# Kernel tuning notes

Measured on AMD Instinct MI355X. Metric: run time of the kernel, lower is better.

The kernel has to match this reference:

```python
import jax, jax.numpy as jnp
import numpy as np

N = 50000        # nodes
E = 800000       # edges (avg degree 16)
F_IN = 128
H = 128
C = 16


def setup_inputs() -> dict:
    key = jax.random.key(0)
    ks = jax.random.split(key, 12)
    x = jax.random.normal(ks[0], (N, F_IN), dtype=jnp.float32)
    edges = jax.random.randint(ks[1], (2, E), 0, N, dtype=jnp.int32)
    dims = [(F_IN, H), (H, H // 2), (H // 2, H // 4), (H // 4, H // 8), (H // 8, C)]
    params = {}
    for i, (di, do) in enumerate(dims):
        params[f"W{i+1}"] = jax.random.normal(ks[2 + 2 * i], (di, do), dtype=jnp.float32) * (1.0 / np.sqrt(di)).astype(np.float32)
        params[f"b{i+1}"] = jax.random.normal(ks[3 + 2 * i], (do,), dtype=jnp.float32) * 0.01
    return {"x": x, "edges": edges, **params}


def reference(x, edges, W1, b1, W2, b2, W3, b3, W4, b4, W5, b5):
    src, dst = edges[0], edges[1]
    ones = jnp.ones((E,), x.dtype)
    # symmetric ('both') normalization with degree clamped to >= 1 (DGL GraphConv default)
    out_deg = jnp.clip(jax.ops.segment_sum(ones, src, num_segments=N), 1.0, None)
    in_deg = jnp.clip(jax.ops.segment_sum(ones, dst, num_segments=N), 1.0, None)
    norm_src = (out_deg ** -0.5)[:, None]   # [N,1]
    norm_dst = (in_deg ** -0.5)[:, None]    # [N,1]

    def graph_conv(h, W, b):
        h = h @ W                                  # dense transform first (out <= in)
        msgs = (h * norm_src)[src]                 # [E, d_out] gather
        agg = jax.ops.segment_sum(msgs, dst, num_segments=N)  # scatter-add SpMM
        return agg * norm_dst + b

    h = x
    for W, b in ((W1, b1), (W2, b2), (W3, b3), (W4, b4), (W5, b5)):
        h = jax.nn.relu(graph_conv(h, W, b))
    return h
```

## Files before the change

kernel.cpp:

```cpp
#include <hip/hip_runtime.h>
#include <hip/hip_bf16.h>


#define THREADS 256
#define HIST_B 256
#define HWORDS 12500
#define RS_BLOCKS 196
#define G1BLKS 1564

typedef __attribute__((ext_vector_type(8))) short short8_t;
typedef __attribute__((ext_vector_type(4))) float float4_t;

__device__ __forceinline__ unsigned short f2bf_rne(float f) {
    unsigned u = __builtin_bit_cast(unsigned, f);
    unsigned r = u + 0x7fffu + ((u >> 16) & 1u);
    return (unsigned short)(r >> 16);
}
__device__ __forceinline__ float bf2f(unsigned short h) {
    return __builtin_bit_cast(float, ((unsigned)h) << 16);
}

template<int K, int NOUT, bool NORM>
__device__ __forceinline__ void gemm_core(const float* __restrict__ A,
                                          const short* lh, const short* ll,
                                          const float* __restrict__ norm,
                                          short* __restrict__ outq,
                                          float* __restrict__ qscale,
                                          int M, int blk, int tid,
                                          int ostride, int ocol0,
                                          int qstride, int qoff) {
    constexpr int Kp  = (K + 31) & ~31;
    constexpr int STR = Kp + 8;
    constexpr int NT  = NOUT / 16;

    const int w    = tid >> 6;
    const int lane = tid & 63;
    const int ln   = lane & 15;
    const int quad = lane >> 4;
    const int row  = blk * 64 + w * 16 + ln;
    const bool rv  = row < M;

    float4_t acc[NT];
#pragma unroll
    for (int i = 0; i < NT; ++i) acc[i] = (float4_t){0.f, 0.f, 0.f, 0.f};

#pragma unroll
    for (int kt = 0; kt < Kp / 32; ++kt) {
        const int k0 = kt * 32 + quad * 8;
        float a[8];
        if (rv && k0 < K) {
            float4 v0 = *(const float4*)&A[(size_t)row * K + k0];
            float4 v1 = *(const float4*)&A[(size_t)row * K + k0 + 4];
            a[0] = v0.x; a[1] = v0.y; a[2] = v0.z; a[3] = v0.w;
            a[4] = v1.x; a[5] = v1.y; a[6] = v1.z; a[7] = v1.w;
        } else {
#pragma unroll
            for (int j = 0; j < 8; ++j) a[j] = 0.f;
        }
        short8_t ahi, alo;
#pragma unroll
        for (int j = 0; j < 8; ++j) {
            unsigned short h = f2bf_rne(a[j]);
            ahi[j] = (short)h;
            alo[j] = (short)f2bf_rne(a[j] - bf2f(h));
        }
#pragma unroll
        for (int nt = 0; nt < NT; ++nt) {
            const int bidx = (nt * 16 + ln) * STR + kt * 32 + quad * 8;
            short8_t bh = *(const short8_t*)&lh[bidx];
            short8_t bl = *(const short8_t*)&ll[bidx];
            acc[nt] = __builtin_amdgcn_mfma_f32_16x16x32_bf16(ahi, bh, acc[nt], 0, 0, 0);
            acc[nt] = __builtin_amdgcn_mfma_f32_16x16x32_bf16(ahi, bl, acc[nt], 0, 0, 0);
            acc[nt] = __builtin_amdgcn_mfma_f32_16x16x32_bf16(alo, bh, acc[nt], 0, 0, 0);
        }
    }

    const int orow = blk * 64 + w * 16 + quad * 4;
#pragma unroll
    for (int i = 0; i < 4; ++i) {
        int r = orow + i;
        float m = 0.f;
#pragma unroll
        for (int nt = 0; nt < NT; ++nt) m = fmaxf(m, fabsf(acc[nt][i]));
#pragma unroll
        for (int off = 1; off < 16; off <<= 1) m = fmaxf(m, __shfl_xor(m, off));
        float s = 1.f;
        if (NORM) s = (r < M) ? norm[r] : 0.f;
        float rowmax = m * s;
        float inv = (rowmax > 0.f) ? (32767.f / rowmax) : 0.f;
        if (r < M) {
            if (ln == 0) qscale[r * qstride + qoff] = rowmax * (1.f / 32767.f);
#pragma unroll
            for (int nt = 0; nt < NT; ++nt)
                outq[(size_t)r * ostride + ocol0 + nt * 16 + ln] =
                    (short)(int)__builtin_rintf(acc[nt][i] * s * inv);
        }
    }
}

__device__ __forceinline__ void conv_one(const float* __restrict__ W, short* __restrict__ hi,
                                         short* __restrict__ lo, int K, int NOUT, int STR, int i) {
    int n = i / STR;
    int kk = i % STR;
    float v = (kk < K) ? W[(size_t)kk * NOUT + n] : 0.f;
    unsigned short h = f2bf_rne(v);
    hi[i] = (short)h;
    lo[i] = (short)f2bf_rne(v - bf2f(h));
}

__global__ __launch_bounds__(THREADS)
void packed0_kernel(const float* __restrict__ x, const float* __restrict__ W1,
                    const float* __restrict__ W2, const float* __restrict__ W3,
                    const float* __restrict__ W4, const float* __restrict__ W5,
                    short* __restrict__ tq, float* __restrict__ qscale2,
                    const int* __restrict__ src, const int* __restrict__ dst,
                    unsigned* __restrict__ p_src, unsigned* __restrict__ p_dst,
                    unsigned char* __restrict__ rank, int* __restrict__ flags,
                    short* w2h, short* w2l, short* w3h, short* w3l,
                    short* w4h, short* w4l, short* w5h, short* w5l,
                    int E, int chunk, int N) {
    __shared__ __align__(16) char smem[50048];
    const int blk = blockIdx.x;
    const int t = threadIdx.x;

    if (blk < G1BLKS) {
        const int h  = blk & 1;
        const int gb = blk >> 1;
        short* lh = (short*)smem;
        short* ll = (short*)smem + 8704;
        for (int j = t; j < 128 * 64; j += THREADS) {
            int kk = j >> 6, n = j & 63;
            float v = W1[kk * 128 + h * 64 + n];
            unsigned short hh = f2bf_rne(v);
            lh[n * 136 + kk] = (short)hh;
            ll[n * 136 + kk] = (short)f2bf_rne(v - bf2f(hh));
        }
        __syncthreads();
        gemm_core<128, 64, false>(x, lh, ll, nullptr, tq, qscale2, N, gb, t,
                                  128, h * 64, 2, h);
    } else if (blk < G1BLKS + 2 * HIST_B) {
        unsigned* bins = (unsigned*)smem;
        const int hb = blk - G1BLKS;
        const bool is_dst = hb < HIST_B;
        const int b = is_dst ? hb : hb - HIST_B;
        const int e0 = b * chunk;
        int e1 = e0 + chunk; if (e1 > E) e1 = E;
        const int* __restrict__ idx = is_dst ? dst : src;
        unsigned* __restrict__ pout = is_dst ? p_dst : p_src;

        for (int w = t; w < HWORDS; w += THREADS) bins[w] = 0;
        __syncthreads();
        for (int e = e0 + t; e < e1; e += THREADS) {
            int d = idx[e];
            unsigned sh = (unsigned)(d & 3) * 8u;
            unsigned old = atomicAdd(&bins[d >> 2], 1u << sh);
            if (is_dst) rank[e] = (unsigned char)((old >> sh) & 0xffu);
        }
        __syncthreads();
        for (int w = t; w < HWORDS; w += THREADS)
            pout[(size_t)b * HWORDS + w] = bins[w];
    } else {
        int cb = blk - G1BLKS - 2 * HIST_B;
        if (cb == 48) {
            flags[t] = 0;
            return;
        }
        int i = cb * THREADS + t;
        if (i < 8704)                        conv_one(W2, w2h, w2l, 128, 64, 136, i);
        else if ((i -= 8704) < 2304)         conv_one(W3, w3h, w3l, 64, 32, 72, i);
        else if ((i -= 2304) < 640)          conv_one(W4, w4h, w4l, 32, 16, 40, i);
        else { i -= 640;                     conv_one(W5, w5h, w5l, 16, 16, 40, i); }
    }
}

__global__ __launch_bounds__(THREADS)
void reduce_scan_kernel(const unsigned* __restrict__ p_src, unsigned* __restrict__ p_dst,
                        float* __restrict__ norm_src, float* __restrict__ norm_dst,
                        float* __restrict__ qscale2, int* __restrict__ row_ptr,
                        int* __restrict__ flags, int N) {
    __shared__ unsigned qd[4][64];
    __shared__ unsigned qs[4][64];
    __shared__ int sscan[64];
    __shared__ int bexcl_sh;
    const int t  = threadIdx.x;
    const int b  = blockIdx.x;
    const int q  = t >> 6;
    const int wl = t & 63;
    const int w  = b * 64 + wl;
    const bool wv = (w < HWORDS);

    unsigned vals[64];
    unsigned dsum = 0, ssum = 0;
    if (wv) {
#pragma unroll
        for (int i = 0; i < 64; ++i) {
            int c = q * 64 + i;
            vals[i] = p_dst[(size_t)c * HWORDS + w];
            dsum += vals[i];
        }
#pragma unroll
        for (int i = 0; i < 64; ++i) {
            int c = q * 64 + i;
            ssum += p_src[(size_t)c * HWORDS + w];
        }
    }
    qd[q][wl] = dsum;
    qs[q][wl] = ssum;
    __syncthreads();

    unsigned off = 0, dfull = 0, sfull = 0;
#pragma unroll
    for (int qq = 0; qq < 4; ++qq) {
        unsigned v = qd[qq][wl];
        if (qq < q) off += v;
        dfull += v;
        sfull += qs[qq][wl];
    }

    if (wv) {
        unsigned run = off;
#pragma unroll
        for (int i = 0; i < 64; ++i) {
            int c = q * 64 + i;
            p_dst[(size_t)c * HWORDS + w] = run;
            run += vals[i];
        }
    }

    int d0 = 0, d1 = 0, d2 = 0, d3 = 0, wdeg = 0;
    if (q == 0) {
        d0 = (int)(dfull & 0xffu); d1 = (int)((dfull >> 8) & 0xffu);
        d2 = (int)((dfull >> 16) & 0xffu); d3 = (int)(dfull >> 24);
        wdeg = d0 + d1 + d2 + d3;
        if (wv) {
#pragma unroll
            for (int l = 0; l < 4; ++l) {
                int node = 4 * w + l;
                int dd = (l == 0) ? d0 : (l == 1) ? d1 : (l == 2) ? d2 : d3;
                int ds = (int)((sfull >> (8 * l)) & 0xffu);
                norm_dst[node] = rsqrtf((float)(dd < 1 ? 1 : dd));
                float ns = rsqrtf((float)(ds < 1 ? 1 : ds));
                norm_src[node] = ns;
                qscale2[2 * node]     *= ns;
                qscale2[2 * node + 1] *= ns;
            }
        }
        sscan[wl] = wv ? wdeg : 0;
    }
    __syncthreads();
    for (int o = 1; o < 64; o <<= 1) {
        int u = 0;
        if (t < 64 && t >= o) u = sscan[t - o];
        __syncthreads();
        if (t < 64) sscan[t] += u;
        __syncthreads();
    }
    const int btotal = sscan[63];

    if (t == 0) atomicExch(&flags[b], btotal + 1);
    if (t < 64) {
        int v = 0;
        for (int p = t; p < b; p += 64) {
            int f;
            do { f = atomicAdd(&flags[p], 0); } while (f == 0);
            v += f - 1;
        }
#pragma unroll
        for (int o = 1; o < 64; o <<= 1) v += __shfl_xor(v, o);
        if (t == 0) bexcl_sh = v;
    }
    __syncthreads();

    if (q == 0 && wv) {
        int pre = bexcl_sh + sscan[wl] - wdeg;
        int n0 = 4 * w;
        row_ptr[n0 + 0] = pre; pre += d0;
        row_ptr[n0 + 1] = pre; pre += d1;
        row_ptr[n0 + 2] = pre; pre += d2;
        row_ptr[n0 + 3] = pre;
    }
    if (b == RS_BLOCKS - 1 && t == 0) row_ptr[N] = bexcl_sh + btotal;
}

__global__ __launch_bounds__(THREADS)
void scatter_kernel(const int* __restrict__ src, const int* __restrict__ dst,
                    const unsigned char* __restrict__ rank,
                    const int* __restrict__ row_ptr, const unsigned* __restrict__ p_dst,
                    int* __restrict__ col, int E, int chunk) {
    const int bc = blockIdx.x >> 1;
    const int hch = (chunk + 1) >> 1;
    const int e0 = bc * chunk;
    int e1 = e0 + chunk; if (e1 > E) e1 = E;
    int s = e0 + (blockIdx.x & 1) * hch;
    int send = s + hch; if (send > e1) send = e1;
    for (int e = s + threadIdx.x; e < send; e += THREADS) {
        int d = dst[e];
        unsigned sh = (unsigned)(d & 3) * 8u;
        unsigned pre = (p_dst[(size_t)bc * HWORDS + (d >> 2)] >> sh) & 0xffu;
        col[row_ptr[d] + (int)pre + (int)rank[e]] = src[e];
    }
}

template<int K, int NOUT>
__global__ __launch_bounds__(THREADS)
void gemm_mfma_kernel(const float* __restrict__ A, const short* __restrict__ wt_hi,
                      const short* __restrict__ wt_lo, const float* __restrict__ norm,
                      short* __restrict__ outq, float* __restrict__ qscale, int M) {
    constexpr int Kp  = (K + 31) & ~31;
    constexpr int STR = Kp + 8;

    __shared__ short lh[NOUT * STR];
    __shared__ short ll[NOUT * STR];

    const int tid = threadIdx.x;
    {
        constexpr int CNT = NOUT * STR / 2;
        const int* gh = (const int*)wt_hi;
        const int* gl = (const int*)wt_lo;
        int* sh = (int*)lh;
        int* sl = (int*)ll;
        for (int i = tid; i < CNT; i += THREADS) { sh[i] = gh[i]; sl[i] = gl[i]; }
    }
    __syncthreads();
    gemm_core<K, NOUT, true>(A, lh, ll, norm, outq, qscale, M, blockIdx.x, tid,
                             NOUT, 0, 1, 0);
}

template<int D, bool QS2>
__global__ __launch_bounds__(THREADS)
void agg_q_kernel(const short* __restrict__ tq, const float* __restrict__ qscale,
                  const int* __restrict__ row_ptr, const int* __restrict__ col,
                  const float* __restrict__ norm_dst, const float* __restrict__ bias,
                  float* __restrict__ out, int N) {
    constexpr int TPN = D / 8;
    constexpr int NPB = THREADS / TPN;
    const int tid  = threadIdx.x;
    const int ln   = tid % TPN;
    const int g    = tid / TPN;
    const int node = blockIdx.x * NPB + g;
    if (node >= N) return;

    const int half = QS2 ? (ln >> 3) : 0;
    const int beg = row_ptr[node];
    const int end = row_ptr[node + 1];

    float acc[8];
#pragma unroll
    for (int c = 0; c < 8; ++c) acc[c] = 0.f;

    auto scl = [&](int s) -> float {
        return QS2 ? qscale[2 * s + half] : qscale[s];
    };

    int j = beg;
    for (; j + 3 < end; j += 4) {
        int s0 = col[j], s1 = col[j + 1], s2 = col[j + 2], s3 = col[j + 3];
        short8_t v0 = *(const short8_t*)&tq[(size_t)s0 * D + ln * 8];
        short8_t v1 = *(const short8_t*)&tq[(size_t)s1 * D + ln * 8];
        short8_t v2 = *(const short8_t*)&tq[(size_t)s2 * D + ln * 8];
        short8_t v3 = *(const short8_t*)&tq[(size_t)s3 * D + ln * 8];
        float c0 = scl(s0), c1 = scl(s1), c2 = scl(s2), c3 = scl(s3);
#pragma unroll
        for (int c = 0; c < 8; ++c)
            acc[c] += (float)v0[c] * c0 + (float)v1[c] * c1
                    + (float)v2[c] * c2 + (float)v3[c] * c3;
    }
    for (; j < end; ++j) {
        int s0 = col[j];
        short8_t v0 = *(const short8_t*)&tq[(size_t)s0 * D + ln * 8];
        float c0 = scl(s0);
#pragma unroll
        for (int c = 0; c < 8; ++c) acc[c] += (float)v0[c] * c0;
    }

    float nd = norm_dst[node];
    float4 b0 = *(const float4*)&bias[ln * 8];
    float4 b1 = *(const float4*)&bias[ln * 8 + 4];
    float4 o0, o1;
    o0.x = fmaxf(acc[0] * nd + b0.x, 0.f);
    o0.y = fmaxf(acc[1] * nd + b0.y, 0.f);
    o0.z = fmaxf(acc[2] * nd + b0.z, 0.f);
    o0.w = fmaxf(acc[3] * nd + b0.w, 0.f);
    o1.x = fmaxf(acc[4] * nd + b1.x, 0.f);
    o1.y = fmaxf(acc[5] * nd + b1.y, 0.f);
    o1.z = fmaxf(acc[6] * nd + b1.z, 0.f);
    o1.w = fmaxf(acc[7] * nd + b1.w, 0.f);
    *(float4*)&out[(size_t)node * D + ln * 8] = o0;
    *(float4*)&out[(size_t)node * D + ln * 8 + 4] = o1;
}

extern "C" void kernel_launch(void* const* d_in, const int* in_sizes, int n_in,
                              void* d_out, int out_size, void* d_ws, size_t ws_size,
                              hipStream_t stream) {
    const float* x     = (const float*)d_in[0];
    const int*   edges = (const int*)d_in[1];
    const float* W1 = (const float*)d_in[2];  const float* b1 = (const float*)d_in[3];
    const float* W2 = (const float*)d_in[4];  const float* b2 = (const float*)d_in[5];
    const float* W3 = (const float*)d_in[6];  const float* b3 = (const float*)d_in[7];
    const float* W4 = (const float*)d_in[8];  const float* b4 = (const float*)d_in[9];
    const float* W5 = (const float*)d_in[10]; const float* b5 = (const float*)d_in[11];

    const int N = in_sizes[0] / 128;
    const int E = in_sizes[1] / 2;
    const int* src = edges;
    const int* dst = edges + E;

    char* ws = (char*)d_ws;
    size_t off = 0;
    auto carve = [&](size_t bytes) -> void* {
        void* p = ws + off;
        off += (bytes + 255) & ~(size_t)255;
        return p;
    };
    short* tq       = (short*)carve((size_t)N * 128 * 2);
    float* hbuf     = (float*)carve((size_t)N * 128 * 4);
    float* norm_src = (float*)carve((size_t)N * 4);
    float* norm_dst = (float*)carve((size_t)N * 4);
    int*   row_ptr  = (int*)carve((size_t)(N + 1) * 4);
    int*   col      = (int*)carve((size_t)E * 4);
    float* qscale   = (float*)carve((size_t)2 * N * 4);
    int*   flags    = (int*)carve((size_t)256 * 4);
    short* wts      = (short*)carve((size_t)24576 * 2);
    unsigned* p_src = (unsigned*)carve((size_t)HIST_B * HWORDS * 4);
    unsigned* p_dst = (unsigned*)carve((size_t)HIST_B * HWORDS * 4);
    unsigned char* rank = (unsigned char*)carve((size_t)E);
    (void)ws_size;

    short* w2h = wts;            short* w2l = w2h + 8704;
    short* w3h = w2l + 8704;     short* w3l = w3h + 2304;
    short* w4h = w3l + 2304;     short* w4l = w4h + 640;
    short* w5h = w4l + 640;      short* w5l = w5h + 640;

    const int chunk = (E + HIST_B - 1) / HIST_B;
    const int gridG = (N + 63) / 64;

    packed0_kernel<<<G1BLKS + 2 * HIST_B + 49, THREADS, 0, stream>>>(
        x, W1, W2, W3, W4, W5, tq, qscale, src, dst, p_src, p_dst, rank, flags,
        w2h, w2l, w3h, w3l, w4h, w4l, w5h, w5l, E, chunk, N);

    reduce_scan_kernel<<<RS_BLOCKS, THREADS, 0, stream>>>(
        p_src, p_dst, norm_src, norm_dst, qscale, row_ptr, flags, N);

    scatter_kernel<<<2 * HIST_B, THREADS, 0, stream>>>(src, dst, rank, row_ptr, p_dst, col, E, chunk);

    agg_q_kernel<128, true><<<(N + 15) / 16, THREADS, 0, stream>>>(tq, qscale, row_ptr, col, norm_dst, b1, hbuf, N);

    gemm_mfma_kernel<128, 64><<<gridG, THREADS, 0, stream>>>(hbuf, w2h, w2l, norm_src, tq, qscale, N);
    agg_q_kernel<64, false><<<(N + 31) / 32, THREADS, 0, stream>>>(tq, qscale, row_ptr, col, norm_dst, b2, hbuf, N);

    gemm_mfma_kernel<64, 32><<<gridG, THREADS, 0, stream>>>(hbuf, w3h, w3l, norm_src, tq, qscale, N);
    agg_q_kernel<32, false><<<(N + 63) / 64, THREADS, 0, stream>>>(tq, qscale, row_ptr, col, norm_dst, b3, hbuf, N);

    gemm_mfma_kernel<32, 16><<<gridG, THREADS, 0, stream>>>(hbuf, w4h, w4l, norm_src, tq, qscale, N);
    agg_q_kernel<16, false><<<(N + 127) / 128, THREADS, 0, stream>>>(tq, qscale, row_ptr, col, norm_dst, b4, hbuf, N);

    gemm_mfma_kernel<16, 16><<<gridG, THREADS, 0, stream>>>(hbuf, w5h, w5l, norm_src, tq, qscale, N);
    agg_q_kernel<16, false><<<(N + 127) / 128, THREADS, 0, stream>>>(tq, qscale, row_ptr, col, norm_dst, b5, (float*)d_out, N);
}
```

Before: 278.8 us.

## Fuse per-layer aggregation with next layer's MFMA GEMM via LDS tile

Each layer's SpMM aggregation (with bias, ReLU and dst norm) now writes its 64-node output tile into shared memory, and the next layer's bf16-split MFMA GEMM consumes it directly. The fp32 hidden buffer round-trip through global memory and four kernel launches go away, with ping-pong quantized buffers replacing the single one. In exchange, aggregation parallelism is tied to 64-node GEMM blocks, which risks lower occupancy from the larger LDS footprint and less latency hiding in the gather.

```diff
diff --git a/kernel.cpp b/kernel.cpp
--- a/kernel.cpp
+++ b/kernel.cpp
@@ -20,19 +20,48 @@
     return __builtin_bit_cast(float, ((unsigned)h) << 16);
 }
 
+template<int NT, bool NORM>
+__device__ __forceinline__ void quant_epilogue(float4_t* acc, const float* __restrict__ norm,
+                                               short* __restrict__ outq, float* __restrict__ qscale,
+                                               int M, int blk, int tid,
+                                               int ostride, int ocol0, int qstride, int qoff) {
+    const int w    = tid >> 6;
+    const int lane = tid & 63;
+    const int ln   = lane & 15;
+    const int quad = lane >> 4;
+    const int orow = blk * 64 + w * 16 + quad * 4;
+#pragma unroll
+    for (int i = 0; i < 4; ++i) {
+        int r = orow + i;
+        float m = 0.f;
+#pragma unroll
+        for (int nt = 0; nt < NT; ++nt) m = fmaxf(m, fabsf(acc[nt][i]));
+#pragma unroll
+        for (int off = 1; off < 16; off <<= 1) m = fmaxf(m, __shfl_xor(m, off));
+        float s = 1.f;
+        if (NORM) s = (r < M) ? norm[r] : 0.f;
+        float rowmax = m * s;
+        float inv = (rowmax > 0.f) ? (32767.f / rowmax) : 0.f;
+        if (r < M) {
+            if (ln == 0) qscale[r * qstride + qoff] = rowmax * (1.f / 32767.f);
+#pragma unroll
+            for (int nt = 0; nt < NT; ++nt)
+                outq[(size_t)r * ostride + ocol0 + nt * 16 + ln] =
+                    (short)(int)__builtin_rintf(acc[nt][i] * s * inv);
+        }
+    }
+}
+
 template<int K, int NOUT, bool NORM>
 __device__ __forceinline__ void gemm_core(const float* __restrict__ A,
                                           const short* lh, const short* ll,
                                           const float* __restrict__ norm,
-                                          short* __restrict__ outq,
-                                          float* __restrict__ qscale,
+                                          short* __restrict__ outq, float* __restrict__ qscale,
                                           int M, int blk, int tid,
-                                          int ostride, int ocol0,
-                                          int qstride, int qoff) {
+                                          int ostride, int ocol0, int qstride, int qoff) {
     constexpr int Kp  = (K + 31) & ~31;
     constexpr int STR = Kp + 8;
     constexpr int NT  = NOUT / 16;
-
     const int w    = tid >> 6;
     const int lane = tid & 63;
     const int ln   = lane & 15;
@@ -74,28 +103,60 @@
             acc[nt] = __builtin_amdgcn_mfma_f32_16x16x32_bf16(alo, bh, acc[nt], 0, 0, 0);
         }
     }
-
-    const int orow = blk * 64 + w * 16 + quad * 4;
-#pragma unroll
-    for (int i = 0; i < 4; ++i) {
-        int r = orow + i;
-        float m = 0.f;
-#pragma unroll
-        for (int nt = 0; nt < NT; ++nt) m = fmaxf(m, fabsf(acc[nt][i]));
-#pragma unroll
-        for (int off = 1; off < 16; off <<= 1) m = fmaxf(m, __shfl_xor(m, off));
-        float s = 1.f;
-        if (NORM) s = (r < M) ? norm[r] : 0.f;
-        float rowmax = m * s;
-        float inv = (rowmax > 0.f) ? (32767.f / rowmax) : 0.f;
-        if (r < M) {
-            if (ln == 0) qscale[r * qstride + qoff] = rowmax * (1.f / 32767.f);
-#pragma unroll
-            for (int nt = 0; nt < NT; ++nt)
-                outq[(size_t)r * ostride + ocol0 + nt * 16 + ln] =
-                    (short)(int)__builtin_rintf(acc[nt][i] * s * inv);
-        }
-    }
+    quant_epilogue<NT, NORM>(acc, norm, outq, qscale, M, blk, tid, ostride, ocol0, qstride, qoff);
+}
+
+template<int K, int NOUT, int DINP>
+__device__ __forceinline__ void gemm_core_lds(const float* As,
+                                              const short* lh, const short* ll,
+                                              const float* __restrict__ norm,
+                                              short* __restrict__ outq, float* __restrict__ qscale,
+                                              int M, int blk, int tid) {
+    constexpr int Kp  = (K + 31) & ~31;
+    constexpr int STR = Kp + 8;
+    constexpr int NT  = NOUT / 16;
+    const int w    = tid >> 6;
+    const int lane = tid & 63;
+    const int ln   = lane & 15;
+    const int quad = lane >> 4;
+    const int rloc = w * 16 + ln;
+    const bool rv  = (blk * 64 + rloc) < M;
+
+    float4_t acc[NT];
+#pragma unroll
+    for (int i = 0; i < NT; ++i) acc[i] = (float4_t){0.f, 0.f, 0.f, 0.f};
+
+#pragma unroll
+    for (int kt = 0; kt < Kp / 32; ++kt) {
+        const int k0 = kt * 32 + quad * 8;
+        float a[8];
+        if (rv && k0 < K) {
+            float4 v0 = *(const float4*)&As[rloc * DINP + k0];
+            float4 v1 = *(const float4*)&As[rloc * DINP + k0 + 4];
+            a[0] = v0.x; a[1] = v0.y; a[2] = v0.z; a[3] = v0.w;
+            a[4] = v1.x; a[5] = v1.y; a[6] = v1.z; a[7] = v1.w;
+        } else {
+#pragma unroll
+            for (int j = 0; j < 8; ++j) a[j] = 0.f;
+        }
+        short8_t ahi, alo;
+#pragma unroll
+        for (int j = 0; j < 8; ++j) {
+            unsigned short h = f2bf_rne(a[j]);
+            ahi[j] = (short)h;
+            alo[j] = (short)f2bf_rne(a[j] - bf2f(h));
+        }
+#pragma unroll
+        for (int nt = 0; nt < NT; ++nt) {
+            const int bidx = (nt * 16 + ln) * STR + kt * 32 + quad * 8;
+            short8_t bh = *(const short8_t*)&lh[bidx];
+            short8_t bl = *(const short8_t*)&ll[bidx];
+            acc[nt] = __builtin_amdgcn_mfma_f32_16x16x32_bf16(ahi, bh, acc[nt], 0, 0, 0);
+            acc[nt] = __builtin_amdgcn_mfma_f32_16x16x32_bf16(ahi, bl, acc[nt], 0, 0, 0);
+            acc[nt] = __builtin_amdgcn_mfma_f32_16x16x32_bf16(alo, bh, acc[nt], 0, 0, 0);
+        }
+    }
+    quant_epilogue<NT, true>(acc, norm, outq, qscale, M, blk, tid, NOUT, 0, 1, 0);
 }
 
 __device__ __forceinline__ void conv_one(const float* __restrict__ W, short* __restrict__ hi,
@@ -301,14 +362,20 @@
     }
 }
 
-template<int K, int NOUT>
+template<int DIN, int NOUT, bool QS2_IN>
 __global__ __launch_bounds__(THREADS)
-void gemm_mfma_kernel(const float* __restrict__ A, const short* __restrict__ wt_hi,
-                      const short* __restrict__ wt_lo, const float* __restrict__ norm,
-                      short* __restrict__ outq, float* __restrict__ qscale, int M) {
-    constexpr int Kp  = (K + 31) & ~31;
-    constexpr int STR = Kp + 8;
-
+void fused_agg_gemm_kernel(const short* __restrict__ tq_in, const float* __restrict__ qs_in,
+                           const int* __restrict__ row_ptr, const int* __restrict__ col,
+                           const float* __restrict__ norm_dst, const float* __restrict__ bias,
+                           const short* __restrict__ wt_hi, const short* __restrict__ wt_lo,
+                           const float* __restrict__ norm_src,
+                           short* __restrict__ tq_out, float* __restrict__ qs_out, int N) {
+    constexpr int Kp   = (DIN + 31) & ~31;
+    constexpr int STR  = Kp + 8;
+    constexpr int DINP = DIN + 4;
+    constexpr int TPN  = DIN / 8;
+
+    __shared__ float As[64 * DINP];
     __shared__ short lh[NOUT * STR];
     __shared__ short ll[NOUT * STR];
 
@@ -321,12 +388,50 @@
         int* sl = (int*)ll;
         for (int i = tid; i < CNT; i += THREADS) { sh[i] = gh[i]; sl[i] = gl[i]; }
     }
+
+    const int ln = tid % TPN;
+    const int half = QS2_IN ? (ln >> 3) : 0;
+    for (int n0 = tid / TPN; n0 < 64; n0 += THREADS / TPN) {
+        const int node = blockIdx.x * 64 + n0;
+        if (node < N) {
+            const int beg = row_ptr[node];
+            const int end = row_ptr[node + 1];
+            float acc[8];
+#pragma unroll
+            for (int c = 0; c < 8; ++c) acc[c] = 0.f;
+            auto scl = [&](int s) -> float { return QS2_IN ? qs_in[2 * s + half] : qs_in[s]; };
+            int j = beg;
+            for (; j + 3 < end; j += 4) {
+                int s0 = col[j], s1 = col[j + 1], s2 = col[j + 2], s3 = col[j + 3];
+                short8_t v0 = *(const short8_t*)&tq_in[(size_t)s0 * DIN + ln * 8];
+                short8_t v1 = *(const short8_t*)&tq_in[(size_t)s1 * DIN + ln * 8];
+                short8_t v2 = *(const short8_t*)&tq_in[(size_t)s2 * DIN + ln * 8];
+                short8_t v3 = *(const short8_t*)&tq_in[(size_t)s3 * DIN + ln * 8];
+                float c0 = scl(s0), c1 = scl(s1), c2 = scl(s2), c3 = scl(s3);
+#pragma unroll
+                for (int c = 0; c < 8; ++c)
+                    acc[c] += (float)v0[c] * c0 + (float)v1[c] * c1
+                            + (float)v2[c] * c2 + (float)v3[c] * c3;
+            }
+            for (; j < end; ++j) {
+                int s0 = col[j];
+                short8_t v0 = *(const short8_t*)&tq_in[(size_t)s0 * DIN + ln * 8];
+                float c0 = scl(s0);
+#pragma unroll
+                for (int c = 0; c < 8; ++c) acc[c] += (float)v0[c] * c0;
+            }
+            float nd = norm_dst[node];
+#pragma unroll
+            for (int c = 0; c < 8; ++c)
+                As[n0 * DINP + ln * 8 + c] = fmaxf(acc[c] * nd + bias[ln * 8 + c], 0.f);
+        }
+    }
     __syncthreads();
-    gemm_core<K, NOUT, true>(A, lh, ll, norm, outq, qscale, M, blockIdx.x, tid,
-                             NOUT, 0, 1, 0);
-}
-
-template<int D, bool QS2>
+
+    gemm_core_lds<DIN, NOUT, DINP>(As, lh, ll, norm_src, tq_out, qs_out, N, blockIdx.x, tid);
+}
+
+template<int D>
 __global__ __launch_bounds__(THREADS)
 void agg_q_kernel(const short* __restrict__ tq, const float* __restrict__ qscale,
                   const int* __restrict__ row_ptr, const int* __restrict__ col,
@@ -340,17 +445,12 @@
     const int node = blockIdx.x * NPB + g;
     if (node >= N) return;
 
-    const int half = QS2 ? (ln >> 3) : 0;
     const int beg = row_ptr[node];
     const int end = row_ptr[node + 1];
 
     float acc[8];
 #pragma unroll
     for (int c = 0; c < 8; ++c) acc[c] = 0.f;
-
-    auto scl = [&](int s) -> float {
-        return QS2 ? qscale[2 * s + half] : qscale[s];
-    };
 
     int j = beg;
     for (; j + 3 < end; j += 4) {
@@ -359,7 +459,7 @@
         short8_t v1 = *(const short8_t*)&tq[(size_t)s1 * D + ln * 8];
         short8_t v2 = *(const short8_t*)&tq[(size_t)s2 * D + ln * 8];
         short8_t v3 = *(const short8_t*)&tq[(size_t)s3 * D + ln * 8];
-        float c0 = scl(s0), c1 = scl(s1), c2 = scl(s2), c3 = scl(s3);
+        float c0 = qscale[s0], c1 = qscale[s1], c2 = qscale[s2], c3 = qscale[s3];
 #pragma unroll
         for (int c = 0; c < 8; ++c)
             acc[c] += (float)v0[c] * c0 + (float)v1[c] * c1
@@ -368,7 +468,7 @@
     for (; j < end; ++j) {
         int s0 = col[j];
         short8_t v0 = *(const short8_t*)&tq[(size_t)s0 * D + ln * 8];
-        float c0 = scl(s0);
+        float c0 = qscale[s0];
 #pragma unroll
         for (int c = 0; c < 8; ++c) acc[c] += (float)v0[c] * c0;
     }
@@ -412,13 +512,14 @@
         off += (bytes + 255) & ~(size_t)255;
         return p;
     };
-    short* tq       = (short*)carve((size_t)N * 128 * 2);
-    float* hbuf     = (float*)carve((size_t)N * 128 * 4);
+    short* tqA      = (short*)carve((size_t)N * 128 * 2);
+    short* tqB      = (short*)carve((size_t)N * 64 * 2);
     float* norm_src = (float*)carve((size_t)N * 4);
     float* norm_dst = (float*)carve((size_t)N * 4);
     int*   row_ptr  = (int*)carve((size_t)(N + 1) * 4);
     int*   col      = (int*)carve((size_t)E * 4);
-    float* qscale   = (float*)carve((size_t)2 * N * 4);
+    float* qsA      = (float*)carve((size_t)2 * N * 4);
+    float* qsB      = (float*)carve((size_t)N * 4);
     int*   flags    = (int*)carve((size_t)256 * 4);
     short* wts      = (short*)carve((size_t)24576 * 2);
     unsigned* p_src = (unsigned*)carve((size_t)HIST_B * HWORDS * 4);
@@ -435,25 +536,23 @@
     const int gridG = (N + 63) / 64;
 
     packed0_kernel<<<G1BLKS + 2 * HIST_B + 49, THREADS, 0, stream>>>(
-        x, W1, W2, W3, W4, W5, tq, qscale, src, dst, p_src, p_dst, rank, flags,
+        x, W1, W2, W3, W4, W5, tqA, qsA, src, dst, p_src, p_dst, rank, flags,
         w2h, w2l, w3h, w3l, w4h, w4l, w5h, w5l, E, chunk, N);
 
     reduce_scan_kernel<<<RS_BLOCKS, THREADS, 0, stream>>>(
-        p_src, p_dst, norm_src, norm_dst, qscale, row_ptr, flags, N);
+        p_src, p_dst, norm_src, norm_dst, qsA, row_ptr, flags, N);
 
     scatter_kernel<<<2 * HIST_B, THREADS, 0, stream>>>(src, dst, rank, row_ptr, p_dst, col, E, chunk);
 
-    agg_q_kernel<128, true><<<(N + 15) / 16, THREADS, 0, stream>>>(tq, qscale, row_ptr, col, norm_dst, b1, hbuf, N);
-
-    gemm_mfma_kernel<128, 64><<<gridG, THREADS, 0, stream>>>(hbuf, w2h, w2l, norm_src, tq, qscale, N);
-    agg_q_kernel<64, false><<<(N + 31) / 32, THREADS, 0, stream>>>(tq, qscale, row_ptr, col, norm_dst, b2, hbuf, N);
-
-    gemm_mfma_kernel<64, 32><<<gridG, THREADS, 0, stream>>>(hbuf, w3h, w3l, norm_src, tq, qscale, N);
-    agg_q_kernel<32, false><<<(N + 63) / 64, THREADS, 0, stream>>>(tq, qscale, row_ptr, col, norm_dst, b3, hbuf, N);
-
-    gemm_mfma_kernel<32, 16><<<gridG, THREADS, 0, stream>>>(hbuf, w4h, w4l, norm_src, tq, qscale, N);
-    agg_q_kernel<16, false><<<(N + 127) / 128, THREADS, 0, stream>>>(tq, qscale, row_ptr, col, norm_dst, b4, hbuf, N);
-
-    gemm_mfma_kernel<16, 16><<<gridG, THREADS, 0, stream>>>(hbuf, w5h, w5l, norm_src, tq, qscale, N);
-    agg_q_kernel<16, false><<<(N + 127) / 128, THREADS, 0, stream>>>(tq, qscale, row_ptr, col, norm_dst, b5, (float*)d_out, N);
-}
+    fused_agg_gemm_kernel<128, 64, true><<<gridG, THREADS, 0, stream>>>(
+        tqA, qsA, row_ptr, col, norm_dst, b1, w2h, w2l, norm_src, tqB, qsB, N);
+    fused_agg_gemm_kernel<64, 32, false><<<gridG, THREADS, 0, stream>>>(
+        tqB, qsB, row_ptr, col, norm_dst, b2, w3h, w3l, norm_src, tqA, qsA, N);
+    fused_agg_gemm_kernel<32, 16, false><<<gridG, THREADS, 0, stream>>>(
+        tqA, qsA, row_ptr, col, norm_dst, b3, w4h, w4l, norm_src, tqB, qsB, N);
+    fused_agg_gemm_kernel<16, 16, false><<<gridG, THREADS, 0, stream>>>(
+        tqB, qsB, row_ptr, col, norm_dst, b4, w5h, w5l, norm_src, tqA, qsA, N);
+
+    agg_q_kernel<16><<<(N + 127) / 128, THREADS, 0, stream>>>(
+        tqA, qsA, row_ptr, col, norm_dst, b5, (float*)d_out, N);
+}
```

Result: slower. 290.7 us (+4.3%).
